# Kernel tuning notes

Measured on AMD Instinct MI355X. Metric: run time of the kernel, lower is better.

## Reference

```python
import jax, jax.numpy as jnp
import numpy as np

B, H, W = 16, 56, 56
CE, CB = 128, 256
NH, WS = 8, 7
HD = CB // NH
N = WS * WS
HID = 4 * CB
EPS = 1e-5


def _rel_pos_index(ws):
    coords = np.stack(np.meshgrid(np.arange(ws), np.arange(ws), indexing='ij')).reshape(2, -1)
    rel = (coords[:, :, None] - coords[:, None, :]).transpose(1, 2, 0).astype(np.int64)
    rel[..., 0] += ws - 1
    rel[..., 1] += ws - 1
    rel[..., 0] *= 2 * ws - 1
    return rel.sum(-1)  # (ws*ws, ws*ws)

RPI = jnp.asarray(_rel_pos_index(WS))


def _ln(x, w, b, axes):
    m = x.mean(axes, keepdims=True)
    v = x.var(axes, keepdims=True)
    return (x - m) * jax.lax.rsqrt(v + EPS) * w + b


def _window_partition(x):  # (B,H,W,C) -> (B*nW, N, C)
    Bx, Hx, Wx, C = x.shape
    x = x.reshape(Bx, Hx // WS, WS, Wx // WS, WS, C)
    return x.transpose(0, 1, 3, 2, 4, 5).reshape(-1, N, C)


def _window_reverse(xw, C):  # (B*nW, N, C) -> (B,H,W,C)
    x = xw.reshape(B, H // WS, W // WS, WS, WS, C)
    return x.transpose(0, 1, 3, 2, 4, 5).reshape(B, H, W, C)


def setup_inputs() -> dict:
    key = jax.random.key(0)
    ks = jax.random.split(key, 12)
    s = 0.02
    return {
        'x_edge': jax.random.normal(ks[0], (B, CE, H, W), jnp.float32),
        'x_body': jax.random.normal(ks[1], (B, H * W, CB), jnp.float32),
        'norm_edge_w': jnp.ones((CE, H, W), jnp.float32),
        'norm_edge_b': jnp.zeros((CE, H, W), jnp.float32),
        'conv_w': jax.random.normal(ks[2], (CB, CE), jnp.float32) * s,
        'norm1_w': jnp.ones((CB,), jnp.float32),
        'norm1_b': jnp.zeros((CB,), jnp.float32),
        'rpb_table': jax.random.normal(ks[3], ((2 * WS - 1) ** 2, NH), jnp.float32) * s,
        'q_w': jax.random.normal(ks[4], (CB, CB), jnp.float32) * s,
        'kv_w': jax.random.normal(ks[5], (2 * CB, CB), jnp.float32) * s,
        'proj_w': jax.random.normal(ks[6], (CB, CB), jnp.float32) * s,
        'proj_b': jnp.zeros((CB,), jnp.float32),
        'norm2_w': jnp.ones((CB,), jnp.float32),
        'norm2_b': jnp.zeros((CB,), jnp.float32),
        'fc1_w': jax.random.normal(ks[7], (HID, CB), jnp.float32) * s,
        'fc1_b': jnp.zeros((HID,), jnp.float32),
        'fc2_w': jax.random.normal(ks[8], (CB, HID), jnp.float32) * s,
        'fc2_b': jnp.zeros((CB,), jnp.float32),
    }


def reference(x_edge, x_body, norm_edge_w, norm_edge_b, conv_w, norm1_w, norm1_b,
              rpb_table, q_w, kv_w, proj_w, proj_b, norm2_w, norm2_b,
              fc1_w, fc1_b, fc2_w, fc2_b):
    x_body_cache = x_body
    scale = HD ** -0.5

    # LayerNorm over (C,H,W) of x_edge, then 1x1 conv (channel mixing), to NHWC
    xe = _ln(x_edge, norm_edge_w, norm_edge_b, axes=(1, 2, 3))  # (B,CE,H,W)
    xe = jnp.einsum('oc,bchw->bhwo', conv_w, xe)                # (B,H,W,CB)

    xb = _ln(x_body, norm1_w, norm1_b, axes=(-1,)).reshape(B, H, W, CB)

    xe_w = _window_partition(xe)  # (Bn,N,CB)
    xb_w = _window_partition(xb)

    q = (xe_w @ q_w.T).reshape(-1, N, NH, HD).transpose(0, 2, 1, 3) * scale  # (Bn,NH,N,HD)
    kv = (xb_w @ kv_w.T).reshape(-1, N, 2, NH, HD).transpose(2, 0, 3, 1, 4)
    k, v = kv[0], kv[1]  # (Bn,NH,N,HD)

    attn = jnp.einsum('bhnd,bhmd->bhnm', q, k)
    bias = rpb_table[RPI.reshape(-1)].reshape(N, N, NH).transpose(2, 0, 1)  # (NH,N,N)
    attn = jax.nn.softmax(attn + bias[None], axis=-1)

    out = jnp.einsum('bhnm,bhmd->bhnd', attn, v).transpose(0, 2, 1, 3).reshape(-1, N, CB)
    out = out @ proj_w.T + proj_b

    x_attn = _window_reverse(out, CB).reshape(B, H * W, CB)
    x = x_body_cache + x_attn

    h = _ln(x, norm2_w, norm2_b, axes=(-1,))
    h = jax.nn.gelu(h @ fc1_w.T + fc1_b, approximate=False) @ fc2_w.T + fc2_b
    x = x + h

    return x.reshape(B, H, W, CB).transpose(0, 3, 1, 2)  # (B,CB,H,W)
```

## Files before the change

kernel.cpp:

```cpp
#include <hip/hip_runtime.h>
#include <hip/hip_bf16.h>
#include <math.h>

#define B_    16
#define CE_   128
#define CB_   256
#define H_    56
#define W_    56
#define NH_   8
#define WS_   7
#define HD_   32
#define NWIN_ 49
#define HW_   3136
#define M_    50176
#define HID_  1024

typedef short bf16x8 __attribute__((ext_vector_type(8)));
typedef float f32x4  __attribute__((ext_vector_type(4)));

__device__ __forceinline__ float waveRedSum(float v) {
#pragma unroll
  for (int off = 32; off; off >>= 1) v += __shfl_xor(v, off, 64);
  return v;
}

__device__ __forceinline__ void load_lds16(const void* g, void* l) {
  __builtin_amdgcn_global_load_lds((__attribute__((address_space(1))) void*)g,
                                   (__attribute__((address_space(3))) void*)l,
                                   16, 0, 0);
}

__global__ void k_stats1(const float* __restrict__ xe, float* __restrict__ part) {
  int blk = blockIdx.x;
  int b = blk >> 6, s = blk & 63;
  const float4* p = (const float4*)(xe + (size_t)b * 401408 + s * 6272);
  float sm = 0.f, s2 = 0.f;
  for (int i = threadIdx.x; i < 1568; i += 256) {
    float4 v = p[i];
    sm += v.x + v.y + v.z + v.w;
    s2 += v.x * v.x + v.y * v.y + v.z * v.z + v.w * v.w;
  }
  sm = waveRedSum(sm); s2 = waveRedSum(s2);
  __shared__ float aux[8];
  int wave = threadIdx.x >> 6, lane = threadIdx.x & 63;
  if (lane == 0) { aux[wave] = sm; aux[4 + wave] = s2; }
  __syncthreads();
  if (threadIdx.x == 0) {
    part[blk * 2]     = aux[0] + aux[1] + aux[2] + aux[3];
    part[blk * 2 + 1] = aux[4] + aux[5] + aux[6] + aux[7];
  }
}

__global__ void k_stats2(const float* __restrict__ part, float* __restrict__ stats) {
  int b = blockIdx.x, lane = threadIdx.x;
  float sm = part[(b * 64 + lane) * 2];
  float s2 = part[(b * 64 + lane) * 2 + 1];
  sm = waveRedSum(sm); s2 = waveRedSum(s2);
  if (lane == 0) {
    float mean = sm / 401408.0f;
    float var  = s2 / 401408.0f - mean * mean;
    stats[b * 2] = mean;
    stats[b * 2 + 1] = rsqrtf(var + 1e-5f);
  }
}

__global__ void k_cast6(const float* __restrict__ s0, const float* __restrict__ s1,
                        const float* __restrict__ s2, const float* __restrict__ s3,
                        const float* __restrict__ s4, const float* __restrict__ s5,
                        __hip_bfloat16* __restrict__ d) {
  size_t i4 = ((size_t)blockIdx.x * 256 + threadIdx.x) * 4;
  if (i4 >= 819200) return;
  const float* src; size_t off;
  if      (i4 < 32768)  { src = s0; off = 0; }
  else if (i4 < 98304)  { src = s1; off = 32768; }
  else if (i4 < 229376) { src = s2; off = 98304; }
  else if (i4 < 294912) { src = s3; off = 229376; }
  else if (i4 < 557056) { src = s4; off = 294912; }
  else                  { src = s5; off = 557056; }
  float4 v = *(const float4*)(src + (i4 - off));
  union { __hip_bfloat16 h[4]; uint2 u; } pk;
  pk.h[0] = __float2bfloat16(v.x);
  pk.h[1] = __float2bfloat16(v.y);
  pk.h[2] = __float2bfloat16(v.z);
  pk.h[3] = __float2bfloat16(v.w);
  *(uint2*)(d + i4) = pk.u;
}

__global__ void k_bias_pre(const float* __restrict__ rpb, float* __restrict__ bp) {
  int blk = blockIdx.x;
  int h = blk >> 4, tile = blk & 15;
  int ti = tile >> 2, tj = tile & 3;
  int lane = threadIdx.x;
  int quad = lane >> 4, lm = lane & 15;
  float4 v;
  float* vp = (float*)&v;
#pragma unroll
  for (int r = 0; r < 4; ++r) {
    int i = ti * 16 + quad * 4 + r;
    int j = tj * 16 + lm;
    float b = -1e30f;
    if (i < 49 && j < 49) {
      int rel = (i / 7 - j / 7 + 6) * 13 + (i % 7 - j % 7 + 6);
      b = rpb[rel * 8 + h];
    }
    vp[r] = b;
  }
  *(float4*)&bp[(size_t)(blk * 64 + lane) * 4] = v;
}

__global__ void k_prep_edge(const float* __restrict__ xe,
                            const float* __restrict__ we,
                            const float* __restrict__ be,
                            const float* __restrict__ stats,
                            __hip_bfloat16* __restrict__ Ae) {
  int wb = blockIdx.x;
  int b = wb >> 6, rem = wb & 63;
  int h0 = (rem >> 3) * 7, w0 = (rem & 7) * 7;
  float mean = stats[b * 2], rstd = stats[b * 2 + 1];
  __shared__ __hip_bfloat16 t[49 * 130];
  for (int idx = threadIdx.x; idx < 128 * 49; idx += 256) {
    int c = idx / 49, p = idx % 49;
    int h = h0 + p / 7, w = w0 + p % 7;
    int off = (c * 56 + h) * 56 + w;
    float v = xe[(size_t)b * 401408 + off];
    t[p * 130 + c] = __float2bfloat16((v - mean) * rstd * we[off] + be[off]);
  }
  __syncthreads();
  __hip_bfloat16* dst = Ae + (size_t)wb * 49 * 128;
  for (int idx = threadIdx.x; idx < 49 * 128; idx += 256) {
    int p = idx >> 7, c = idx & 127;
    dst[idx] = t[p * 130 + c];
  }
}

template <bool PERM>
__global__ void k_ln_rows(const float* __restrict__ x,
                          const float* __restrict__ w,
                          const float* __restrict__ bia,
                          __hip_bfloat16* __restrict__ out) {
  int row = blockIdx.x * 4 + (threadIdx.x >> 6);
  int lane = threadIdx.x & 63;
  float4 xv = *(const float4*)(x + (size_t)row * 256 + lane * 4);
  float s  = xv.x + xv.y + xv.z + xv.w;
  float s2 = xv.x * xv.x + xv.y * xv.y + xv.z * xv.z + xv.w * xv.w;
  s = waveRedSum(s); s2 = waveRedSum(s2);
  float mean = s * (1.0f / 256.0f);
  float var  = s2 * (1.0f / 256.0f) - mean * mean;
  float rstd = rsqrtf(var + 1e-5f);
  int orow = row;
  if (PERM) {
    int b = row / 3136, hw = row % 3136;
    int h = hw / 56, ww = hw % 56;
    orow = (b * 64 + (h / 7) * 8 + (ww / 7)) * 49 + (h % 7) * 7 + (ww % 7);
  }
  float4 wv = *(const float4*)(w + lane * 4);
  float4 bv = *(const float4*)(bia + lane * 4);
  union { __hip_bfloat16 h[4]; uint2 u; } pk;
  pk.h[0] = __float2bfloat16((xv.x - mean) * rstd * wv.x + bv.x);
  pk.h[1] = __float2bfloat16((xv.y - mean) * rstd * wv.y + bv.y);
  pk.h[2] = __float2bfloat16((xv.z - mean) * rstd * wv.z + bv.z);
  pk.h[3] = __float2bfloat16((xv.w - mean) * rstd * wv.w + bv.w);
  *(uint2*)(out + (size_t)orow * 256 + lane * 4) = pk.u;
}

template <int EPI>
__launch_bounds__(256)
__global__ void gemm_bt(const __hip_bfloat16* __restrict__ A,
                        const __hip_bfloat16* __restrict__ Bw,
                        int M, int N, int K,
                        __hip_bfloat16* __restrict__ outb,
                        float* __restrict__ outf,
                        const float* __restrict__ bias,
                        const float* __restrict__ resid,
                        float scale) {
  __shared__ __hip_bfloat16 As[4 * 128 * 8];
  __shared__ __hip_bfloat16 Bs[4 * 128 * 8];
  const int tid  = threadIdx.x;
  const int lane = tid & 63;
  const int wave = tid >> 6;
  const int quad = lane >> 4;
  const int lm   = lane & 15;
  const int wm   = (wave & 1) << 6;
  const int wn   = (wave >> 1) << 6;
  const int n0   = blockIdx.x * 128;
  const int m0   = blockIdx.y * 128;

  const int rh = (wave & 1) * 64;
  const int qw = wave >> 1;
  const __hip_bfloat16* Arow = A  + (size_t)(m0 + rh + lane) * K;
  const __hip_bfloat16* Brow = Bw + (size_t)(n0 + rh + lane) * K;

  f32x4 acc[4][4];
#pragma unroll
  for (int i = 0; i < 4; ++i)
#pragma unroll
    for (int j = 0; j < 4; ++j)
#pragma unroll
      for (int r = 0; r < 4; ++r) acc[i][j][r] = 0.f;

  for (int k0 = 0; k0 < K; k0 += 32) {
#pragma unroll
    for (int p = 0; p < 2; ++p) {
      int q = qw + 2 * p;
      load_lds16(Arow + k0 + q * 8, &As[(q * 128 + rh) * 8]);
      load_lds16(Brow + k0 + q * 8, &Bs[(q * 128 + rh) * 8]);
    }
    __syncthreads();
    bf16x8 af[4], bfr[4];
#pragma unroll
    for (int i = 0; i < 4; ++i)
      af[i] = *(const bf16x8*)&As[(quad * 128 + wm + i * 16 + lm) * 8];
#pragma unroll
    for (int j = 0; j < 4; ++j)
      bfr[j] = *(const bf16x8*)&Bs[(quad * 128 + wn + j * 16 + lm) * 8];
#pragma unroll
    for (int i = 0; i < 4; ++i)
#pragma unroll
      for (int j = 0; j < 4; ++j)
        acc[i][j] = __builtin_amdgcn_mfma_f32_16x16x32_bf16(af[i], bfr[j], acc[i][j], 0, 0, 0);
    __syncthreads();
  }

#pragma unroll
  for (int i = 0; i < 4; ++i) {
#pragma unroll
    for (int j = 0; j < 4; ++j) {
#pragma unroll
      for (int r = 0; r < 4; ++r) {
        int gm = m0 + wm + i * 16 + quad * 4 + r;
        int gn = n0 + wn + j * 16 + lm;
        float v = acc[i][j][r];
        if constexpr (EPI == 0) {
          outb[(size_t)gm * N + gn] = __float2bfloat16(v);
        } else if constexpr (EPI == 1) {
          outb[(size_t)gm * N + gn] = __float2bfloat16(v * scale);
        } else if constexpr (EPI == 2) {
          int wb = gm / 49, nn = gm % 49;
          int b = wb >> 6, rem = wb & 63;
          int h = (rem >> 3) * 7 + nn / 7, w = (rem & 7) * 7 + nn % 7;
          size_t nat = (size_t)(b * 3136 + h * 56 + w);
          outf[nat * 256 + gn] = v + bias[gn] + resid[nat * 256 + gn];
        } else if constexpr (EPI == 3) {
          float x = v + bias[gn];
          outb[(size_t)gm * N + gn] =
              __float2bfloat16(0.5f * x * (1.0f + erff(x * 0.70710678118654752f)));
        } else {
          outf[(size_t)gm * N + gn] = v + bias[gn] + resid[(size_t)gm * 256 + gn];
        }
      }
    }
  }
}

__launch_bounds__(64)
__global__ void k_attn_mfma(const __hip_bfloat16* __restrict__ qb,
                            const __hip_bfloat16* __restrict__ kvb,
                            const float* __restrict__ bp,
                            __hip_bfloat16* __restrict__ ob) {
  int wb = blockIdx.x >> 3;
  int h  = blockIdx.x & 7;
  __shared__ __align__(16) __hip_bfloat16 lds[7424];
  __hip_bfloat16* Qs = lds;
  __hip_bfloat16* Ks = lds + 2560;
  __hip_bfloat16* Vt = lds + 5120;
  __hip_bfloat16* Ps = lds;
  const int lane = threadIdx.x;
  const int quad = lane >> 4, lm = lane & 15;

  const __hip_bfloat16 zb = __float2bfloat16(0.f);
  for (int i = lane; i < 600; i += 64) { Qs[1960 + i] = zb; Ks[1960 + i] = zb; }
  {
    uint4 z; z.x = z.y = z.z = z.w = 0u;
    for (int i = lane; i < 288; i += 64) ((uint4*)Vt)[i] = z;
  }
  {
    int t = lane >> 2, p = lane & 3;
#pragma unroll
    for (int pass = 0; pass < 4; ++pass, t += 16) {
      if (t < 49) {
        size_t rq = (size_t)(wb * 49 + t);
        uint4 qv = *(const uint4*)(qb + rq * 256 + h * 32 + p * 8);
        *(uint4*)&Qs[t * 40 + p * 8] = qv;
        uint4 kv = *(const uint4*)(kvb + rq * 512 + h * 32 + p * 8);
        *(uint4*)&Ks[t * 40 + p * 8] = kv;
        union { uint4 u; __hip_bfloat16 e[8]; } vv;
        vv.u = *(const uint4*)(kvb + rq * 512 + 256 + h * 32 + p * 8);
#pragma unroll
        for (int i = 0; i < 8; ++i) Vt[(p * 8 + i) * 72 + t] = vv.e[i];
      }
    }
  }
  __builtin_amdgcn_s_waitcnt(0);

  bf16x8 qf[4], kf[4];
#pragma unroll
  for (int i = 0; i < 4; ++i) qf[i] = *(const bf16x8*)&Qs[(i * 16 + lm) * 40 + quad * 8];
#pragma unroll
  for (int j = 0; j < 4; ++j) kf[j] = *(const bf16x8*)&Ks[(j * 16 + lm) * 40 + quad * 8];
  f32x4 s[4][4];
#pragma unroll
  for (int i = 0; i < 4; ++i)
#pragma unroll
    for (int j = 0; j < 4; ++j) {
      f32x4 z4; z4[0] = z4[1] = z4[2] = z4[3] = 0.f;
      s[i][j] = __builtin_amdgcn_mfma_f32_16x16x32_bf16(qf[i], kf[j], z4, 0, 0, 0);
    }
#pragma unroll
  for (int ti = 0; ti < 4; ++ti)
#pragma unroll
    for (int tj = 0; tj < 4; ++tj) {
      f32x4 b = *(const f32x4*)&bp[(size_t)(((h * 4 + ti) * 4 + tj) * 64 + lane) * 4];
      s[ti][tj] += b;
    }
  float mrow[4][4], srow[4][4];
#pragma unroll
  for (int ti = 0; ti < 4; ++ti)
#pragma unroll
    for (int r = 0; r < 4; ++r)
      mrow[ti][r] = fmaxf(fmaxf(s[ti][0][r], s[ti][1][r]), fmaxf(s[ti][2][r], s[ti][3][r]));
#pragma unroll
  for (int mask = 1; mask <= 8; mask <<= 1)
#pragma unroll
    for (int ti = 0; ti < 4; ++ti)
#pragma unroll
      for (int r = 0; r < 4; ++r)
        mrow[ti][r] = fmaxf(mrow[ti][r], __shfl_xor(mrow[ti][r], mask, 64));
#pragma unroll
  for (int ti = 0; ti < 4; ++ti)
#pragma unroll
    for (int tj = 0; tj < 4; ++tj)
#pragma unroll
      for (int r = 0; r < 4; ++r)
        s[ti][tj][r] = __expf(s[ti][tj][r] - mrow[ti][r]);
#pragma unroll
  for (int ti = 0; ti < 4; ++ti)
#pragma unroll
    for (int r = 0; r < 4; ++r)
      srow[ti][r] = s[ti][0][r] + s[ti][1][r] + s[ti][2][r] + s[ti][3][r];
#pragma unroll
  for (int mask = 1; mask <= 8; mask <<= 1)
#pragma unroll
    for (int ti = 0; ti < 4; ++ti)
#pragma unroll
      for (int r = 0; r < 4; ++r)
        srow[ti][r] += __shfl_xor(srow[ti][r], mask, 64);
  float inv[4][4];
#pragma unroll
  for (int ti = 0; ti < 4; ++ti)
#pragma unroll
    for (int r = 0; r < 4; ++r)
      inv[ti][r] = 1.0f / srow[ti][r];

#pragma unroll
  for (int ti = 0; ti < 4; ++ti)
#pragma unroll
    for (int tj = 0; tj < 4; ++tj)
#pragma unroll
      for (int r = 0; r < 4; ++r)
        Ps[(ti * 16 + quad * 4 + r) * 72 + tj * 16 + lm] = __float2bfloat16(s[ti][tj][r]);
  __builtin_amdgcn_s_waitcnt(0);

  f32x4 o[4][2];
#pragma unroll
  for (int mt = 0; mt < 4; ++mt)
#pragma unroll
    for (int nt = 0; nt < 2; ++nt)
#pragma unroll
      for (int r = 0; r < 4; ++r) o[mt][nt][r] = 0.f;
#pragma unroll
  for (int kq = 0; kq < 2; ++kq) {
    bf16x8 pa[4], vb[2];
#pragma unroll
    for (int mt = 0; mt < 4; ++mt)
      pa[mt] = *(const bf16x8*)&Ps[(mt * 16 + lm) * 72 + kq * 32 + quad * 8];
#pragma unroll
    for (int nt = 0; nt < 2; ++nt)
      vb[nt] = *(const bf16x8*)&Vt[(nt * 16 + lm) * 72 + kq * 32 + quad * 8];
#pragma unroll
    for (int mt = 0; mt < 4; ++mt)
#pragma unroll
      for (int nt = 0; nt < 2; ++nt)
        o[mt][nt] = __builtin_amdgcn_mfma_f32_16x16x32_bf16(pa[mt], vb[nt], o[mt][nt], 0, 0, 0);
  }
#pragma unroll
  for (int mt = 0; mt < 4; ++mt)
#pragma unroll
    for (int r = 0; r < 4; ++r) {
      int row = mt * 16 + quad * 4 + r;
      if (row < 49) {
#pragma unroll
        for (int nt = 0; nt < 2; ++nt)
          ob[(size_t)(wb * 49 + row) * 256 + h * 32 + nt * 16 + lm] =
              __float2bfloat16(o[mt][nt][r] * inv[mt][r]);
      }
    }
}

__global__ void k_transpose(const float* __restrict__ y, float* __restrict__ out) {
  __shared__ float t[32][33];
  int bb = blockIdx.z;
  int hw0 = blockIdx.x * 32;
  int o0 = blockIdx.y * 32;
  int tx = threadIdx.x, ty = threadIdx.y;
#pragma unroll
  for (int r = 0; r < 4; ++r)
    t[ty + r * 8][tx] = y[(size_t)(bb * 3136 + hw0 + ty + r * 8) * 256 + o0 + tx];
  __syncthreads();
#pragma unroll
  for (int r = 0; r < 4; ++r)
    out[(size_t)(bb * 256 + o0 + ty + r * 8) * 3136 + hw0 + tx] = t[tx][ty + r * 8];
}

extern "C" void kernel_launch(void* const* d_in, const int* in_sizes, int n_in,
                              void* d_out, int out_size, void* d_ws, size_t ws_size,
                              hipStream_t stream) {
  const float* x_edge = (const float*)d_in[0];
  const float* x_body = (const float*)d_in[1];
  const float* ne_w   = (const float*)d_in[2];
  const float* ne_b   = (const float*)d_in[3];
  const float* conv_w = (const float*)d_in[4];
  const float* n1_w   = (const float*)d_in[5];
  const float* n1_b   = (const float*)d_in[6];
  const float* rpb    = (const float*)d_in[7];
  const float* q_w    = (const float*)d_in[8];
  const float* kv_w   = (const float*)d_in[9];
  const float* proj_w = (const float*)d_in[10];
  const float* proj_b = (const float*)d_in[11];
  const float* n2_w   = (const float*)d_in[12];
  const float* n2_b   = (const float*)d_in[13];
  const float* fc1_w  = (const float*)d_in[14];
  const float* fc1_b  = (const float*)d_in[15];
  const float* fc2_w  = (const float*)d_in[16];
  const float* fc2_b  = (const float*)d_in[17];
  float* out = (float*)d_out;
  (void)in_sizes; (void)n_in; (void)out_size; (void)ws_size;

  const size_t SZ_Ae    = (size_t)M_ * 128 * 2;
  const size_t SZ_bf256 = (size_t)M_ * 256 * 2;
  const size_t SZ_bf512 = (size_t)M_ * 512 * 2;
  const size_t SZ_h1    = (size_t)M_ * 1024 * 2;

  char* ws = (char*)d_ws;
  __hip_bfloat16* Wb = (__hip_bfloat16*)ws;
  float* part  = (float*)(ws + 1638400);
  float* stats = (float*)(ws + 1638400 + 8192);
  float* biasp = (float*)(ws + 1638400 + 8192 + 256);
  char*  P     = ws + 1638400 + 8192 + 256 + 131072;
  __hip_bfloat16* w_conv = Wb;
  __hip_bfloat16* w_q    = Wb + 32768;
  __hip_bfloat16* w_kv   = Wb + 98304;
  __hip_bfloat16* w_proj = Wb + 229376;
  __hip_bfloat16* w_fc1  = Wb + 294912;
  __hip_bfloat16* w_fc2  = Wb + 557056;
  __hip_bfloat16* Ae    = (__hip_bfloat16*)(P);
  __hip_bfloat16* xbn   = (__hip_bfloat16*)(P + SZ_Ae);
  __hip_bfloat16* xec   = (__hip_bfloat16*)(P + SZ_Ae + SZ_bf256);
  __hip_bfloat16* qb    = (__hip_bfloat16*)(P + SZ_Ae + 2 * SZ_bf256);
  __hip_bfloat16* kvb   = (__hip_bfloat16*)(P + SZ_Ae + 3 * SZ_bf256);
  __hip_bfloat16* attnb = (__hip_bfloat16*)(P + SZ_Ae + 3 * SZ_bf256 + SZ_bf512);
  __hip_bfloat16* h1 = (__hip_bfloat16*)(P);
  char* tail         = P + ((SZ_h1 + 1024 * 1024) & ~(size_t)1023);
  __hip_bfloat16* xn = (__hip_bfloat16*)tail;
  float*          yb = (float*)tail;
  float*          xf = (float*)d_out;

  const float qscale = 0.17677669529663687f;

  k_cast6<<<800, 256, 0, stream>>>(conv_w, q_w, kv_w, proj_w, fc1_w, fc2_w, Wb);
  k_bias_pre<<<128, 64, 0, stream>>>(rpb, biasp);
  k_stats1<<<1024, 256, 0, stream>>>(x_edge, part);
  k_stats2<<<16, 64, 0, stream>>>(part, stats);
  k_prep_edge<<<1024, 256, 0, stream>>>(x_edge, ne_w, ne_b, stats, Ae);
  k_ln_rows<true><<<M_ / 4, 256, 0, stream>>>(x_body, n1_w, n1_b, xbn);
  gemm_bt<0><<<dim3(2, 392), 256, 0, stream>>>(Ae, w_conv, M_, 256, 128, xec, nullptr, nullptr, nullptr, 0.f);
  gemm_bt<1><<<dim3(2, 392), 256, 0, stream>>>(xec, w_q, M_, 256, 256, qb, nullptr, nullptr, nullptr, qscale);
  gemm_bt<0><<<dim3(4, 392), 256, 0, stream>>>(xbn, w_kv, M_, 512, 256, kvb, nullptr, nullptr, nullptr, 0.f);
  k_attn_mfma<<<8192, 64, 0, stream>>>(qb, kvb, biasp, attnb);
  gemm_bt<2><<<dim3(2, 392), 256, 0, stream>>>(attnb, w_proj, M_, 256, 256, nullptr, xf, proj_b, x_body, 0.f);
  k_ln_rows<false><<<M_ / 4, 256, 0, stream>>>(xf, n2_w, n2_b, xn);
  gemm_bt<3><<<dim3(8, 392), 256, 0, stream>>>(xn, w_fc1, M_, 1024, 256, h1, nullptr, fc1_b, nullptr, 0.f);
  gemm_bt<4><<<dim3(2, 392), 256, 0, stream>>>(h1, w_fc2, M_, 256, 1024, nullptr, yb, fc2_b, xf, 0.f);
  k_transpose<<<dim3(98, 8, 16), dim3(32, 8), 0, stream>>>(yb, out);
}
```

Measured before the change: 561.9 us.

## Fold conv into Q weights, remap GEMM block order, use tanh GELU

Precomputes the product of the q and conv weights with the softmax scale folded in, so the edge branch does one GEMM instead of two and skips the xec intermediate. GEMM blocks now use a 1D grid remapped into XCD-strided row bands to improve L2 locality. The epilogue computes the row address once per row. The erf-based GELU is replaced with the tanh approximation using __expf, which differs numerically from the exact GELU in the reference.

```diff
diff --git a/kernel.cpp b/kernel.cpp
--- a/kernel.cpp
+++ b/kernel.cpp
@@ -86,6 +86,16 @@
   *(uint2*)(d + i4) = pk.u;
 }
 
+__global__ void k_wqc(const float* __restrict__ qw, const float* __restrict__ cw,
+                      __hip_bfloat16* __restrict__ wqc) {
+  int o2 = blockIdx.x, c = threadIdx.x;
+  float acc = 0.f;
+#pragma unroll 4
+  for (int o = 0; o < 256; ++o)
+    acc += qw[o2 * 256 + o] * cw[o * 128 + c];
+  wqc[o2 * 128 + c] = __float2bfloat16(acc * 0.17677669529663687f);
+}
+
 __global__ void k_bias_pre(const float* __restrict__ rpb, float* __restrict__ bp) {
   int blk = blockIdx.x;
   int h = blk >> 4, tile = blk & 15;
@@ -163,7 +173,7 @@
   *(uint2*)(out + (size_t)orow * 256 + lane * 4) = pk.u;
 }
 
-template <int EPI>
+template <int EPI, int NX>
 __launch_bounds__(256)
 __global__ void gemm_bt(const __hip_bfloat16* __restrict__ A,
                         const __hip_bfloat16* __restrict__ Bw,
@@ -171,8 +181,7 @@
                         __hip_bfloat16* __restrict__ outb,
                         float* __restrict__ outf,
                         const float* __restrict__ bias,
-                        const float* __restrict__ resid,
-                        float scale) {
+                        const float* __restrict__ resid) {
   __shared__ __hip_bfloat16 As[4 * 128 * 8];
   __shared__ __hip_bfloat16 Bs[4 * 128 * 8];
   const int tid  = threadIdx.x;
@@ -182,8 +191,11 @@
   const int lm   = lane & 15;
   const int wm   = (wave & 1) << 6;
   const int wn   = (wave >> 1) << 6;
-  const int n0   = blockIdx.x * 128;
-  const int m0   = blockIdx.y * 128;
+  const int lin  = blockIdx.x;
+  const int slot = lin >> 3;
+  const int band = (lin & 7) * 49 + slot / NX;
+  const int n0   = (slot % NX) * 128;
+  const int m0   = band * 128;
 
   const int rh = (wave & 1) * 64;
   const int qw = wave >> 1;
@@ -224,28 +236,33 @@
 #pragma unroll
   for (int i = 0; i < 4; ++i) {
 #pragma unroll
-    for (int j = 0; j < 4; ++j) {
-#pragma unroll
-      for (int r = 0; r < 4; ++r) {
-        int gm = m0 + wm + i * 16 + quad * 4 + r;
+    for (int r = 0; r < 4; ++r) {
+      int gm = m0 + wm + i * 16 + quad * 4 + r;
+      size_t rowbase;
+      if constexpr (EPI == 2) {
+        int wb = gm / 49, nn = gm % 49;
+        int b = wb >> 6, rem = wb & 63;
+        int h = (rem >> 3) * 7 + nn / 7, w = (rem & 7) * 7 + nn % 7;
+        rowbase = (size_t)(b * 3136 + h * 56 + w) * 256;
+      } else {
+        rowbase = (size_t)gm * N;
+      }
+#pragma unroll
+      for (int j = 0; j < 4; ++j) {
         int gn = n0 + wn + j * 16 + lm;
         float v = acc[i][j][r];
         if constexpr (EPI == 0) {
-          outb[(size_t)gm * N + gn] = __float2bfloat16(v);
-        } else if constexpr (EPI == 1) {
-          outb[(size_t)gm * N + gn] = __float2bfloat16(v * scale);
+          outb[rowbase + gn] = __float2bfloat16(v);
         } else if constexpr (EPI == 2) {
-          int wb = gm / 49, nn = gm % 49;
-          int b = wb >> 6, rem = wb & 63;
-          int h = (rem >> 3) * 7 + nn / 7, w = (rem & 7) * 7 + nn % 7;
-          size_t nat = (size_t)(b * 3136 + h * 56 + w);
-          outf[nat * 256 + gn] = v + bias[gn] + resid[nat * 256 + gn];
+          outf[rowbase + gn] = v + bias[gn] + resid[rowbase + gn];
         } else if constexpr (EPI == 3) {
           float x = v + bias[gn];
-          outb[(size_t)gm * N + gn] =
-              __float2bfloat16(0.5f * x * (1.0f + erff(x * 0.70710678118654752f)));
+          float y = 0.7978845608028654f * (x + 0.044715f * x * x * x);
+          float e = __expf(2.0f * y);
+          float th = 1.0f - 2.0f / (e + 1.0f);
+          outb[rowbase + gn] = __float2bfloat16(0.5f * x * (1.0f + th));
         } else {
-          outf[(size_t)gm * N + gn] = v + bias[gn] + resid[(size_t)gm * 256 + gn];
+          outf[rowbase + gn] = v + bias[gn] + resid[rowbase + gn];
         }
       }
     }
@@ -441,44 +458,40 @@
   const size_t SZ_h1    = (size_t)M_ * 1024 * 2;
 
   char* ws = (char*)d_ws;
-  __hip_bfloat16* Wb = (__hip_bfloat16*)ws;
+  __hip_bfloat16* Wb  = (__hip_bfloat16*)ws;
   float* part  = (float*)(ws + 1638400);
   float* stats = (float*)(ws + 1638400 + 8192);
   float* biasp = (float*)(ws + 1638400 + 8192 + 256);
-  char*  P     = ws + 1638400 + 8192 + 256 + 131072;
-  __hip_bfloat16* w_conv = Wb;
-  __hip_bfloat16* w_q    = Wb + 32768;
+  __hip_bfloat16* wqc = (__hip_bfloat16*)(ws + 1638400 + 8192 + 256 + 131072);
+  char*  P     = ws + 1638400 + 8192 + 256 + 131072 + 65536;
   __hip_bfloat16* w_kv   = Wb + 98304;
   __hip_bfloat16* w_proj = Wb + 229376;
   __hip_bfloat16* w_fc1  = Wb + 294912;
   __hip_bfloat16* w_fc2  = Wb + 557056;
   __hip_bfloat16* Ae    = (__hip_bfloat16*)(P);
   __hip_bfloat16* xbn   = (__hip_bfloat16*)(P + SZ_Ae);
-  __hip_bfloat16* xec   = (__hip_bfloat16*)(P + SZ_Ae + SZ_bf256);
-  __hip_bfloat16* qb    = (__hip_bfloat16*)(P + SZ_Ae + 2 * SZ_bf256);
-  __hip_bfloat16* kvb   = (__hip_bfloat16*)(P + SZ_Ae + 3 * SZ_bf256);
-  __hip_bfloat16* attnb = (__hip_bfloat16*)(P + SZ_Ae + 3 * SZ_bf256 + SZ_bf512);
+  __hip_bfloat16* qb    = (__hip_bfloat16*)(P + SZ_Ae + SZ_bf256);
+  __hip_bfloat16* kvb   = (__hip_bfloat16*)(P + SZ_Ae + 2 * SZ_bf256);
+  __hip_bfloat16* attnb = (__hip_bfloat16*)(P + SZ_Ae + 2 * SZ_bf256 + SZ_bf512);
   __hip_bfloat16* h1 = (__hip_bfloat16*)(P);
   char* tail         = P + ((SZ_h1 + 1024 * 1024) & ~(size_t)1023);
   __hip_bfloat16* xn = (__hip_bfloat16*)tail;
   float*          yb = (float*)tail;
   float*          xf = (float*)d_out;
 
-  const float qscale = 0.17677669529663687f;
-
   k_cast6<<<800, 256, 0, stream>>>(conv_w, q_w, kv_w, proj_w, fc1_w, fc2_w, Wb);
+  k_wqc<<<256, 128, 0, stream>>>(q_w, conv_w, wqc);
   k_bias_pre<<<128, 64, 0, stream>>>(rpb, biasp);
   k_stats1<<<1024, 256, 0, stream>>>(x_edge, part);
   k_stats2<<<16, 64, 0, stream>>>(part, stats);
   k_prep_edge<<<1024, 256, 0, stream>>>(x_edge, ne_w, ne_b, stats, Ae);
   k_ln_rows<true><<<M_ / 4, 256, 0, stream>>>(x_body, n1_w, n1_b, xbn);
-  gemm_bt<0><<<dim3(2, 392), 256, 0, stream>>>(Ae, w_conv, M_, 256, 128, xec, nullptr, nullptr, nullptr, 0.f);
-  gemm_bt<1><<<dim3(2, 392), 256, 0, stream>>>(xec, w_q, M_, 256, 256, qb, nullptr, nullptr, nullptr, qscale);
-  gemm_bt<0><<<dim3(4, 392), 256, 0, stream>>>(xbn, w_kv, M_, 512, 256, kvb, nullptr, nullptr, nullptr, 0.f);
+  gemm_bt<0, 2><<<784, 256, 0, stream>>>(Ae, wqc, M_, 256, 128, qb, nullptr, nullptr, nullptr);
+  gemm_bt<0, 4><<<1568, 256, 0, stream>>>(xbn, w_kv, M_, 512, 256, kvb, nullptr, nullptr, nullptr);
   k_attn_mfma<<<8192, 64, 0, stream>>>(qb, kvb, biasp, attnb);
-  gemm_bt<2><<<dim3(2, 392), 256, 0, stream>>>(attnb, w_proj, M_, 256, 256, nullptr, xf, proj_b, x_body, 0.f);
+  gemm_bt<2, 2><<<784, 256, 0, stream>>>(attnb, w_proj, M_, 256, 256, nullptr, xf, proj_b, x_body);
   k_ln_rows<false><<<M_ / 4, 256, 0, stream>>>(xf, n2_w, n2_b, xn);
-  gemm_bt<3><<<dim3(8, 392), 256, 0, stream>>>(xn, w_fc1, M_, 1024, 256, h1, nullptr, fc1_b, nullptr, 0.f);
-  gemm_bt<4><<<dim3(2, 392), 256, 0, stream>>>(h1, w_fc2, M_, 256, 1024, nullptr, yb, fc2_b, xf, 0.f);
+  gemm_bt<3, 8><<<3136, 256, 0, stream>>>(xn, w_fc1, M_, 1024, 256, h1, nullptr, fc1_b, nullptr);
+  gemm_bt<4, 2><<<784, 256, 0, stream>>>(h1, w_fc2, M_, 256, 1024, nullptr, yb, fc2_b, xf);
   k_transpose<<<dim3(98, 8, 16), dim3(32, 8), 0, stream>>>(yb, out);
 }
```

New measurement: 545.3 us. 1.03x faster.
